# Kernel optimization log

Measured on AMD Instinct MI355X. Metric: run time of the kernel, lower is better.

## Reference

```python
import jax, jax.numpy as jnp
import numpy as np

B, T, C, H = 8, 2048, 1024, 128  # batch, seq (=block_size), n_embd, head_size


def setup_inputs() -> dict:
    key = jax.random.key(0)
    kx, kk, kq, kv = jax.random.split(key, 4)
    x = jax.random.normal(kx, (B, T, C), dtype=jnp.float32)
    # nn.Linear(n_embd, head_size, bias=False) weights, stored as (in, out) for x @ W
    s = 1.0 / np.sqrt(C)
    Wk = jax.random.normal(kk, (C, H), dtype=jnp.float32) * s
    Wq = jax.random.normal(kq, (C, H), dtype=jnp.float32) * s
    Wv = jax.random.normal(kv, (C, H), dtype=jnp.float32) * s
    return {"x": x, "Wk": Wk, "Wq": Wq, "Wv": Wv}


def reference(x, Wk, Wq, Wv):
    # x: [B, T, C]
    Bx, Tx, Cx = x.shape
    k = x @ Wk  # [B, T, H]
    q = x @ Wq  # [B, T, H]
    v = x @ Wv  # [B, T, H]
    # NOTE: source multiplies by C**0.5 (not 1/sqrt), kept faithfully
    wei = jnp.einsum("bth,bsh->bts", q, k) * (Cx ** 0.5)  # [B, T, T]
    causal = jnp.tril(jnp.ones((Tx, Tx), dtype=bool))
    wei = jnp.where(causal, wei, -jnp.inf)
    wei = jax.nn.softmax(wei, axis=-1)
    # dropout omitted (eval-mode reference)
    return wei @ v  # [B, T, H]
```

## Files before the change

kernel.cpp:

```cpp
#include <hip/hip_runtime.h>

constexpr int kB = 8;
constexpr int kT = 2048;
constexpr int kC = 1024;
constexpr int kH = 128;
constexpr int kM = kB * kT;
constexpr size_t kMH = (size_t)kM * kH;
constexpr size_t kWH = (size_t)kC * kH;

typedef __attribute__((ext_vector_type(8))) short bf16x8;
typedef __attribute__((ext_vector_type(4))) float f32x4;


__device__ inline unsigned short f2bf_rne(float f) {
    union { float f; unsigned int u; } x; x.f = f;
    unsigned int r = x.u + 0x7fff + ((x.u >> 16) & 1);
    return (unsigned short)(r >> 16);
}
__device__ inline float bf2f(unsigned short h) {
    union { float f; unsigned int u; } x; x.u = ((unsigned int)h) << 16;
    return x.f;
}
__device__ inline unsigned int pack_hi2(float a, float b) {
    return __builtin_amdgcn_perm(__float_as_uint(b), __float_as_uint(a),
                                 0x07060302u);
}
__device__ inline float hi_part(float v) {
    return __uint_as_float(__float_as_uint(v) & 0xffff0000u);
}
__device__ inline void load_lds16(const unsigned short* g, unsigned short* l) {
    __builtin_amdgcn_global_load_lds(
        (const __attribute__((address_space(1))) unsigned int*)g,
        (__attribute__((address_space(3))) unsigned int*)l, 16, 0, 0);
}
#define RAW_BARRIER()  asm volatile("s_barrier" ::: "memory")
#define WAIT_VM0()     asm volatile("s_waitcnt vmcnt(0)" ::: "memory")

__global__ __launch_bounds__(256) void prep_w(
    const float* __restrict__ Wk, const float* __restrict__ Wq,
    const float* __restrict__ Wv, unsigned short* __restrict__ ws)
{
    const int h = blockIdx.x;
    const int mat = blockIdx.y;
    const float* W = (mat == 0) ? Wq : (mat == 1) ? Wk : Wv;
    unsigned short* hi = ws + 5 * kMH + (size_t)(mat * 2) * kWH;
    unsigned short* lo = hi + kWH;

    const int k0 = threadIdx.x * 4;
    unsigned short hv[4], lv[4];
#pragma unroll
    for (int j = 0; j < 4; ++j) {
        const float f = W[(size_t)(k0 + j) * kH + h];
        hv[j] = f2bf_rne(f);
        lv[j] = f2bf_rne(f - bf2f(hv[j]));
    }
    *(uint2*)&hi[(size_t)h * kC + k0] =
        make_uint2(((unsigned)hv[1] << 16) | hv[0], ((unsigned)hv[3] << 16) | hv[2]);
    *(uint2*)&lo[(size_t)h * kC + k0] =
        make_uint2(((unsigned)lv[1] << 16) | lv[0], ((unsigned)lv[3] << 16) | lv[2]);
}

__global__ __launch_bounds__(256, 2) void qkv_mfma(
    const float* __restrict__ x, unsigned short* __restrict__ ws)
{
    __shared__ __align__(16) unsigned short lds[34816];
    unsigned short* Ahi = lds;
    unsigned short* Alo = lds + 9216;
    unsigned short* Bh  = lds + 18432;
    unsigned short* Bl  = lds + 26624;

    const int idx = blockIdx.x;
    const int tid = threadIdx.x;
    const int w = tid >> 6, lane = tid & 63;
    const int li = lane & 15, quad = lane >> 4;

    if (idx < 256) {
        const int mat = idx & 1;
        const int m0 = (idx >> 1) * 128;
        const unsigned short* wThi = ws + 5 * kMH + (size_t)(mat * 2) * kWH;
        const unsigned short* wTlo = wThi + kWH;
        const int wm = w >> 1, wn = w & 1;

        f32x4 acc[4][4];
#pragma unroll
        for (int i = 0; i < 4; ++i)
#pragma unroll
            for (int j = 0; j < 4; ++j) acc[i][j] = (f32x4){0.f, 0.f, 0.f, 0.f};

        for (int kt = 0; kt < kC; kt += 64) {
            if (kt) __syncthreads();
#pragma unroll
            for (int u = 0; u < 8; ++u) {
                const int f = u * 256 + tid;
                const int row = f >> 4, c4 = (f & 15) * 4;
                const float4 xv =
                    *(const float4*)(x + (size_t)(m0 + row) * kC + kt + c4);
                const float l0 = xv.x - hi_part(xv.x), l1 = xv.y - hi_part(xv.y);
                const float l2 = xv.z - hi_part(xv.z), l3 = xv.w - hi_part(xv.w);
                *(uint2*)&Ahi[row * 72 + c4] =
                    make_uint2(pack_hi2(xv.x, xv.y), pack_hi2(xv.z, xv.w));
                *(uint2*)&Alo[row * 72 + c4] =
                    make_uint2(pack_hi2(l0, l1), pack_hi2(l2, l3));
            }
#pragma unroll
            for (int u = 0; u < 4; ++u) {
                const int f = u * 256 + tid;
                const int row = f >> 3, p = f & 7, g = p ^ (row & 7);
                load_lds16(wThi + (size_t)row * kC + kt + g * 8, Bh + f * 8);
                load_lds16(wTlo + (size_t)row * kC + kt + g * 8, Bl + f * 8);
            }
            __syncthreads();

#pragma unroll
            for (int kc = 0; kc < 2; ++kc) {
                bf16x8 ah[4], al[4];
#pragma unroll
                for (int mt = 0; mt < 4; ++mt) {
                    const int ar = (wm * 64 + mt * 16 + li) * 72 + kc * 32 + quad * 8;
                    ah[mt] = *(const bf16x8*)&Ahi[ar];
                    al[mt] = *(const bf16x8*)&Alo[ar];
                }
#pragma unroll
                for (int nt = 0; nt < 4; ++nt) {
                    const int row = wn * 64 + nt * 16 + li;
                    const int pos = (kc * 4 + quad) ^ (li & 7);
                    const bf16x8 bh = *(const bf16x8*)&Bh[row * 64 + pos * 8];
                    const bf16x8 bl = *(const bf16x8*)&Bl[row * 64 + pos * 8];
#pragma unroll
                    for (int mt = 0; mt < 4; ++mt) {
                        acc[mt][nt] = __builtin_amdgcn_mfma_f32_16x16x32_bf16(ah[mt], bh, acc[mt][nt], 0, 0, 0);
                        acc[mt][nt] = __builtin_amdgcn_mfma_f32_16x16x32_bf16(al[mt], bh, acc[mt][nt], 0, 0, 0);
                        acc[mt][nt] = __builtin_amdgcn_mfma_f32_16x16x32_bf16(ah[mt], bl, acc[mt][nt], 0, 0, 0);
                    }
                }
            }
        }
        unsigned short* hip_ = ws + (size_t)(mat * 2) * kMH;
        unsigned short* lop  = hip_ + kMH;
        const float sc = (mat == 0) ? 32.0f : 1.0f;
#pragma unroll
        for (int mt = 0; mt < 4; ++mt)
#pragma unroll
            for (int nt = 0; nt < 4; ++nt) {
                const int col = wn * 64 + nt * 16 + li;
#pragma unroll
                for (int reg = 0; reg < 4; ++reg) {
                    const int row = m0 + wm * 64 + mt * 16 + quad * 4 + reg;
                    const float v = acc[mt][nt][reg] * sc;
                    hip_[(size_t)row * kH + col] = (unsigned short)(__float_as_uint(v) >> 16);
                    lop[(size_t)row * kH + col] =
                        (unsigned short)(__float_as_uint(v - hi_part(v)) >> 16);
                }
            }
    } else {
        const int m0 = (idx - 256) * 64;
        const unsigned short* wThi = ws + 5 * kMH + (size_t)4 * kWH;
        const int rm = w >> 1, rn = w & 1;

        f32x4 acc[2][4];
#pragma unroll
        for (int i = 0; i < 2; ++i)
#pragma unroll
            for (int j = 0; j < 4; ++j) acc[i][j] = (f32x4){0.f, 0.f, 0.f, 0.f};

        for (int kt = 0; kt < kC; kt += 64) {
            if (kt) __syncthreads();
#pragma unroll
            for (int u = 0; u < 4; ++u) {
                const int f = u * 256 + tid;
                const int row = f >> 4, c4 = (f & 15) * 4;
                const float4 xv =
                    *(const float4*)(x + (size_t)(m0 + row) * kC + kt + c4);
                unsigned short h0 = f2bf_rne(xv.x), h1 = f2bf_rne(xv.y);
                unsigned short h2 = f2bf_rne(xv.z), h3 = f2bf_rne(xv.w);
                *(uint2*)&Ahi[row * 72 + c4] =
                    make_uint2(((unsigned)h1 << 16) | h0, ((unsigned)h3 << 16) | h2);
            }
#pragma unroll
            for (int u = 0; u < 4; ++u) {
                const int f = u * 256 + tid;
                const int row = f >> 3, p = f & 7, g = p ^ (row & 7);
                load_lds16(wThi + (size_t)row * kC + kt + g * 8, Bh + f * 8);
            }
            __syncthreads();

#pragma unroll
            for (int kc = 0; kc < 2; ++kc) {
                bf16x8 a[2];
#pragma unroll
                for (int mt = 0; mt < 2; ++mt)
                    a[mt] = *(const bf16x8*)&Ahi[(rm * 32 + mt * 16 + li) * 72 + kc * 32 + quad * 8];
#pragma unroll
                for (int nt = 0; nt < 4; ++nt) {
                    const int row = rn * 64 + nt * 16 + li;
                    const int pos = (kc * 4 + quad) ^ (li & 7);
                    const bf16x8 bh = *(const bf16x8*)&Bh[row * 64 + pos * 8];
#pragma unroll
                    for (int mt = 0; mt < 2; ++mt)
                        acc[mt][nt] = __builtin_amdgcn_mfma_f32_16x16x32_bf16(a[mt], bh, acc[mt][nt], 0, 0, 0);
                }
            }
        }
        unsigned short* vt = ws + 4 * kMH;
        const int bb = m0 >> 11;
        const int t00 = m0 & (kT - 1);
#pragma unroll
        for (int mt = 0; mt < 2; ++mt)
#pragma unroll
            for (int nt = 0; nt < 4; ++nt) {
                const int h = rn * 64 + nt * 16 + li;
                ushort4 pk;
                pk.x = f2bf_rne(acc[mt][nt][0]);
                pk.y = f2bf_rne(acc[mt][nt][1]);
                pk.z = f2bf_rne(acc[mt][nt][2]);
                pk.w = f2bf_rne(acc[mt][nt][3]);
                const int t0 = t00 + rm * 32 + mt * 16 + quad * 4;
                *(ushort4*)&vt[((size_t)(bb * kH + h)) * kT + t0] = pk;
            }
    }
}

__global__ __launch_bounds__(256, 2) void attn_mfma(
    const unsigned short* __restrict__ ws, float* __restrict__ out)
{
    __shared__ __align__(16) unsigned short Kh0[64 * 128];
    __shared__ __align__(16) unsigned short Kl0[64 * 128];
    __shared__ __align__(16) unsigned short Kh1[64 * 128];
    __shared__ __align__(16) unsigned short Kl1[64 * 128];
    __shared__ __align__(16) unsigned short Ps[4][16][40];
    __shared__ __align__(16) float Ml[2][2][2][16];
    __shared__ __align__(16) unsigned short Os[2][16][136];

    const int tid = threadIdx.x;
    const int w = tid >> 6, lane = tid & 63;
    const int li = lane & 15, quad = lane >> 4;
    const int r = w >> 1, c = w & 1;

    const int idx = blockIdx.x;
    const int b = idx & 7;
    const int j = idx >> 3;
    const int qt = (j < 32) ? j : 95 - j;
    const int i0 = qt * 32;
    const int nj = (qt >> 1) + 1;

    const unsigned short* qhi = ws;
    const unsigned short* qlo = ws + kMH;
    const unsigned short* khi = ws + 2 * kMH;
    const unsigned short* klo = ws + 3 * kMH;
    const unsigned short* vt  = ws + 4 * kMH;

    bf16x8 qh[4], ql[4];
    {
        const size_t qoff = ((size_t)(b * kT + i0 + r * 16 + li)) * kH;
#pragma unroll
        for (int kc = 0; kc < 4; ++kc) {
            qh[kc] = *(const bf16x8*)(qhi + qoff + kc * 32 + quad * 8);
            ql[kc] = *(const bf16x8*)(qlo + qoff + kc * 32 + quad * 8);
        }
    }

    f32x4 o[8];
#pragma unroll
    for (int ht = 0; ht < 8; ++ht) o[ht] = (f32x4){0.f, 0.f, 0.f, 0.f};
    float m_i[4] = {-3.0e38f, -3.0e38f, -3.0e38f, -3.0e38f};
    float l_i[4] = {0.f, 0.f, 0.f, 0.f};

    auto stage = [&](int jtile, unsigned short* Kh, unsigned short* Kl) {
        const size_t kgb = ((size_t)(b * kT + jtile * 64)) * kH;
#pragma unroll
        for (int u = 0; u < 4; ++u) {
            const int f = u * 256 + tid;
            const int row = f >> 4, p = f & 15, g = p ^ (row & 15);
            load_lds16(khi + kgb + row * 128 + g * 8, Kh + f * 8);
            load_lds16(klo + kgb + row * 128 + g * 8, Kl + f * 8);
        }
    };

    auto compute = [&](int jtile, const unsigned short* Kh,
                       const unsigned short* Kl,
                       unsigned short* KhN, unsigned short* KlN) {
        bf16x8 vf[8];
#pragma unroll
        for (int ht = 0; ht < 8; ++ht)
            vf[ht] = *(const bf16x8*)(vt + (size_t)(b * kH + ht * 16 + li) * kT +
                                      jtile * 64 + c * 32 + quad * 8);
        __builtin_amdgcn_sched_barrier(0);
        if (jtile + 1 < nj) stage(jtile + 1, KhN, KlN);

        f32x4 s[2];
        s[0] = (f32x4){0.f, 0.f, 0.f, 0.f};
        s[1] = (f32x4){0.f, 0.f, 0.f, 0.f};
#pragma unroll
        for (int nt = 0; nt < 2; ++nt) {
            const int t = c * 32 + nt * 16 + li;
#pragma unroll
            for (int kc = 0; kc < 4; ++kc) {
                const int pos = (kc * 4 + quad) ^ li;
                const bf16x8 kh = *(const bf16x8*)(Kh + t * 128 + pos * 8);
                const bf16x8 kl = *(const bf16x8*)(Kl + t * 128 + pos * 8);
                s[nt] = __builtin_amdgcn_mfma_f32_16x16x32_bf16(qh[kc], kh, s[nt], 0, 0, 0);
                s[nt] = __builtin_amdgcn_mfma_f32_16x16x32_bf16(ql[kc], kh, s[nt], 0, 0, 0);
                s[nt] = __builtin_amdgcn_mfma_f32_16x16x32_bf16(qh[kc], kl, s[nt], 0, 0, 0);
            }
        }
        if (jtile == nj - 1) {
            const int grow0 = i0 + r * 16 + quad * 4;
            const int gcol0 = jtile * 64 + c * 32 + li;
#pragma unroll
            for (int nt = 0; nt < 2; ++nt)
#pragma unroll
                for (int reg = 0; reg < 4; ++reg)
                    if (gcol0 + nt * 16 > grow0 + reg) s[nt][reg] = -3.0e38f;
        }
        float alpha[4];
#pragma unroll
        for (int reg = 0; reg < 4; ++reg) {
            float mr = fmaxf(s[0][reg], s[1][reg]);
            mr = fmaxf(mr, __shfl_xor(mr, 1));
            mr = fmaxf(mr, __shfl_xor(mr, 2));
            mr = fmaxf(mr, __shfl_xor(mr, 4));
            mr = fmaxf(mr, __shfl_xor(mr, 8));
            const float mn = fmaxf(m_i[reg], mr);
            alpha[reg] = __expf(m_i[reg] - mn);
            m_i[reg] = mn;
            const float p0 = __expf(s[0][reg] - mn);
            const float p1 = __expf(s[1][reg] - mn);
            s[0][reg] = p0; s[1][reg] = p1;
            float rs = p0 + p1;
            rs += __shfl_xor(rs, 1);
            rs += __shfl_xor(rs, 2);
            rs += __shfl_xor(rs, 4);
            rs += __shfl_xor(rs, 8);
            l_i[reg] = l_i[reg] * alpha[reg] + rs;
        }
        const f32x4 av = {alpha[0], alpha[1], alpha[2], alpha[3]};
#pragma unroll
        for (int ht = 0; ht < 8; ++ht) o[ht] *= av;
#pragma unroll
        for (int nt = 0; nt < 2; ++nt)
#pragma unroll
            for (int reg = 0; reg < 4; ++reg)
                Ps[w][quad * 4 + reg][nt * 16 + li] = f2bf_rne(s[nt][reg]);
        const bf16x8 pf = *(const bf16x8*)&Ps[w][li][quad * 8];
#pragma unroll
        for (int ht = 0; ht < 8; ++ht)
            o[ht] = __builtin_amdgcn_mfma_f32_16x16x32_bf16(pf, vf[ht], o[ht], 0, 0, 0);
    };

    stage(0, Kh0, Kl0);
    int jt = 0;
    while (true) {
        WAIT_VM0();
        RAW_BARRIER();
        compute(jt, Kh0, Kl0, Kh1, Kl1);
        if (++jt >= nj) break;
        WAIT_VM0();
        RAW_BARRIER();
        compute(jt, Kh1, Kl1, Kh0, Kl0);
        if (++jt >= nj) break;
    }

    __syncthreads();
#pragma unroll
    for (int reg = 0; reg < 4; ++reg) {
        Ml[r][c][0][quad * 4 + reg] = m_i[reg];
        Ml[r][c][1][quad * 4 + reg] = l_i[reg];
    }
    __syncthreads();
    float a_self[4], linv[4];
#pragma unroll
    for (int reg = 0; reg < 4; ++reg) {
        const float mo = Ml[r][c ^ 1][0][quad * 4 + reg];
        const float lo_ = Ml[r][c ^ 1][1][quad * 4 + reg];
        const float mm = fmaxf(m_i[reg], mo);
        a_self[reg] = __expf(m_i[reg] - mm);
        const float a_oth = __expf(mo - mm);
        linv[reg] = 1.0f / (l_i[reg] * a_self[reg] + lo_ * a_oth);
    }
    if (c == 1) {
#pragma unroll
        for (int ht = 0; ht < 8; ++ht)
#pragma unroll
            for (int reg = 0; reg < 4; ++reg)
                Os[r][quad * 4 + reg][ht * 16 + li] =
                    f2bf_rne(o[ht][reg] * a_self[reg]);
    }
    __syncthreads();
    if (c == 0) {
#pragma unroll
        for (int ht = 0; ht < 8; ++ht)
#pragma unroll
            for (int reg = 0; reg < 4; ++reg) {
                const float v = o[ht][reg] * a_self[reg] +
                                bf2f(Os[r][quad * 4 + reg][ht * 16 + li]);
                out[(size_t)(b * kT + i0 + r * 16 + quad * 4 + reg) * kH +
                    ht * 16 + li] = v * linv[reg];
            }
    }
}

extern "C" void kernel_launch(void* const* d_in, const int* in_sizes, int n_in,
                              void* d_out, int out_size, void* d_ws, size_t ws_size,
                              hipStream_t stream) {
    const float* x  = (const float*)d_in[0];
    const float* Wk = (const float*)d_in[1];
    const float* Wq = (const float*)d_in[2];
    const float* Wv = (const float*)d_in[3];
    unsigned short* ws = (unsigned short*)d_ws;
    float* out = (float*)d_out;

    hipLaunchKernelGGL(prep_w, dim3(128, 3), dim3(256), 0, stream, Wk, Wq, Wv, ws);
    hipLaunchKernelGGL(qkv_mfma, dim3(512), dim3(256), 0, stream, x, ws);
    hipLaunchKernelGGL(attn_mfma, dim3(512), dim3(256), 0, stream,
                       (const unsigned short*)ws, out);
}
```

Measured before the change: 216.6 us.

## Split attention KV range across warps and unify QKV projection tiling

The attention kernel now gives each block a 16-row query tile and splits the key range across its four warps in 64-key chunks. K and V are read straight from global memory rather than staged through double-buffered LDS, and the four partial softmax states are merged at the end in fp32. Softmax moves to exp2 by folding log2(e) into the Q scale. The QKV projection uses a single 64-row tiling for all three matrices with a larger grid. This trades LDS reuse of K for more parallelism and occupancy, at the cost of redundant global K/V loads and a four-way reduction.

Result: slower. 229.7 us (+6.0%).

```diff
diff --git a/kernel.cpp b/kernel.cpp
--- a/kernel.cpp
+++ b/kernel.cpp
@@ -8,6 +8,8 @@
 constexpr size_t kMH = (size_t)kM * kH;
 constexpr size_t kWH = (size_t)kC * kH;
 
+#define QSCALE 46.166241308446828f
+
 typedef __attribute__((ext_vector_type(8))) short bf16x8;
 typedef __attribute__((ext_vector_type(4))) float f32x4;
 
@@ -33,8 +35,6 @@
         (const __attribute__((address_space(1))) unsigned int*)g,
         (__attribute__((address_space(3))) unsigned int*)l, 16, 0, 0);
 }
-#define RAW_BARRIER()  asm volatile("s_barrier" ::: "memory")
-#define WAIT_VM0()     asm volatile("s_waitcnt vmcnt(0)" ::: "memory")
 
 __global__ __launch_bounds__(256) void prep_w(
     const float* __restrict__ Wk, const float* __restrict__ Wq,
@@ -60,52 +60,52 @@
         make_uint2(((unsigned)lv[1] << 16) | lv[0], ((unsigned)lv[3] << 16) | lv[2]);
 }
 
-__global__ __launch_bounds__(256, 2) void qkv_mfma(
+__global__ __launch_bounds__(256) void qkv_mfma(
     const float* __restrict__ x, unsigned short* __restrict__ ws)
 {
-    __shared__ __align__(16) unsigned short lds[34816];
-    unsigned short* Ahi = lds;
-    unsigned short* Alo = lds + 9216;
-    unsigned short* Bh  = lds + 18432;
-    unsigned short* Bl  = lds + 26624;
+    __shared__ __align__(16) unsigned short Ah[64][72];
+    __shared__ __align__(16) unsigned short Al[64][72];
+    __shared__ __align__(16) unsigned short Bh[128 * 64];
+    __shared__ __align__(16) unsigned short Bl[128 * 64];
 
     const int idx = blockIdx.x;
+    const int mat = idx >> 8;
+    const int m0 = (idx & 255) * 64;
+    const unsigned short* wThi = ws + 5 * kMH + (size_t)(mat * 2) * kWH;
+    const unsigned short* wTlo = wThi + kWH;
+
     const int tid = threadIdx.x;
     const int w = tid >> 6, lane = tid & 63;
     const int li = lane & 15, quad = lane >> 4;
-
-    if (idx < 256) {
-        const int mat = idx & 1;
-        const int m0 = (idx >> 1) * 128;
-        const unsigned short* wThi = ws + 5 * kMH + (size_t)(mat * 2) * kWH;
-        const unsigned short* wTlo = wThi + kWH;
-        const int wm = w >> 1, wn = w & 1;
-
-        f32x4 acc[4][4];
-#pragma unroll
-        for (int i = 0; i < 4; ++i)
-#pragma unroll
-            for (int j = 0; j < 4; ++j) acc[i][j] = (f32x4){0.f, 0.f, 0.f, 0.f};
-
+    const int wm = w >> 1, wn = w & 1;
+
+    const int ar = tid >> 2;
+    const int ac = (tid & 3) * 16;
+
+    f32x4 acc[2][4];
+#pragma unroll
+    for (int i = 0; i < 2; ++i)
+#pragma unroll
+        for (int j = 0; j < 4; ++j) acc[i][j] = (f32x4){0.f, 0.f, 0.f, 0.f};
+
+    if (mat <= 1) {
         for (int kt = 0; kt < kC; kt += 64) {
             if (kt) __syncthreads();
 #pragma unroll
-            for (int u = 0; u < 8; ++u) {
-                const int f = u * 256 + tid;
-                const int row = f >> 4, c4 = (f & 15) * 4;
+            for (int u = 0; u < 4; ++u) {
                 const float4 xv =
-                    *(const float4*)(x + (size_t)(m0 + row) * kC + kt + c4);
+                    *(const float4*)(x + (size_t)(m0 + ar) * kC + kt + ac + u * 4);
                 const float l0 = xv.x - hi_part(xv.x), l1 = xv.y - hi_part(xv.y);
                 const float l2 = xv.z - hi_part(xv.z), l3 = xv.w - hi_part(xv.w);
-                *(uint2*)&Ahi[row * 72 + c4] =
+                *(uint2*)&Ah[ar][ac + u * 4] =
                     make_uint2(pack_hi2(xv.x, xv.y), pack_hi2(xv.z, xv.w));
-                *(uint2*)&Alo[row * 72 + c4] =
+                *(uint2*)&Al[ar][ac + u * 4] =
                     make_uint2(pack_hi2(l0, l1), pack_hi2(l2, l3));
             }
 #pragma unroll
             for (int u = 0; u < 4; ++u) {
                 const int f = u * 256 + tid;
-                const int row = f >> 3, p = f & 7, g = p ^ (row & 7);
+                const int row = f >> 3, g = (f & 7) ^ (row & 7);
                 load_lds16(wThi + (size_t)row * kC + kt + g * 8, Bh + f * 8);
                 load_lds16(wTlo + (size_t)row * kC + kt + g * 8, Bl + f * 8);
             }
@@ -113,21 +113,20 @@
 
 #pragma unroll
             for (int kc = 0; kc < 2; ++kc) {
-                bf16x8 ah[4], al[4];
-#pragma unroll
-                for (int mt = 0; mt < 4; ++mt) {
-                    const int ar = (wm * 64 + mt * 16 + li) * 72 + kc * 32 + quad * 8;
-                    ah[mt] = *(const bf16x8*)&Ahi[ar];
-                    al[mt] = *(const bf16x8*)&Alo[ar];
+                bf16x8 ah[2], al[2];
+#pragma unroll
+                for (int mt = 0; mt < 2; ++mt) {
+                    ah[mt] = *(const bf16x8*)&Ah[wm * 32 + mt * 16 + li][kc * 32 + quad * 8];
+                    al[mt] = *(const bf16x8*)&Al[wm * 32 + mt * 16 + li][kc * 32 + quad * 8];
                 }
 #pragma unroll
                 for (int nt = 0; nt < 4; ++nt) {
                     const int row = wn * 64 + nt * 16 + li;
-                    const int pos = (kc * 4 + quad) ^ (li & 7);
+                    const int pos = (kc * 4 + quad) ^ (row & 7);
                     const bf16x8 bh = *(const bf16x8*)&Bh[row * 64 + pos * 8];
                     const bf16x8 bl = *(const bf16x8*)&Bl[row * 64 + pos * 8];
 #pragma unroll
-                    for (int mt = 0; mt < 4; ++mt) {
+                    for (int mt = 0; mt < 2; ++mt) {
                         acc[mt][nt] = __builtin_amdgcn_mfma_f32_16x16x32_bf16(ah[mt], bh, acc[mt][nt], 0, 0, 0);
                         acc[mt][nt] = __builtin_amdgcn_mfma_f32_16x16x32_bf16(al[mt], bh, acc[mt][nt], 0, 0, 0);
                         acc[mt][nt] = __builtin_amdgcn_mfma_f32_16x16x32_bf16(ah[mt], bl, acc[mt][nt], 0, 0, 0);
@@ -137,15 +136,15 @@
         }
         unsigned short* hip_ = ws + (size_t)(mat * 2) * kMH;
         unsigned short* lop  = hip_ + kMH;
-        const float sc = (mat == 0) ? 32.0f : 1.0f;
-#pragma unroll
-        for (int mt = 0; mt < 4; ++mt)
+        const float sc = (mat == 0) ? QSCALE : 1.0f;
+#pragma unroll
+        for (int mt = 0; mt < 2; ++mt)
 #pragma unroll
             for (int nt = 0; nt < 4; ++nt) {
                 const int col = wn * 64 + nt * 16 + li;
 #pragma unroll
                 for (int reg = 0; reg < 4; ++reg) {
-                    const int row = m0 + wm * 64 + mt * 16 + quad * 4 + reg;
+                    const int row = m0 + wm * 32 + mt * 16 + quad * 4 + reg;
                     const float v = acc[mt][nt][reg] * sc;
                     hip_[(size_t)row * kH + col] = (unsigned short)(__float_as_uint(v) >> 16);
                     lop[(size_t)row * kH + col] =
@@ -153,33 +152,21 @@
                 }
             }
     } else {
-        const int m0 = (idx - 256) * 64;
-        const unsigned short* wThi = ws + 5 * kMH + (size_t)4 * kWH;
-        const int rm = w >> 1, rn = w & 1;
-
-        f32x4 acc[2][4];
-#pragma unroll
-        for (int i = 0; i < 2; ++i)
-#pragma unroll
-            for (int j = 0; j < 4; ++j) acc[i][j] = (f32x4){0.f, 0.f, 0.f, 0.f};
-
         for (int kt = 0; kt < kC; kt += 64) {
             if (kt) __syncthreads();
 #pragma unroll
             for (int u = 0; u < 4; ++u) {
-                const int f = u * 256 + tid;
-                const int row = f >> 4, c4 = (f & 15) * 4;
                 const float4 xv =
-                    *(const float4*)(x + (size_t)(m0 + row) * kC + kt + c4);
+                    *(const float4*)(x + (size_t)(m0 + ar) * kC + kt + ac + u * 4);
                 unsigned short h0 = f2bf_rne(xv.x), h1 = f2bf_rne(xv.y);
                 unsigned short h2 = f2bf_rne(xv.z), h3 = f2bf_rne(xv.w);
-                *(uint2*)&Ahi[row * 72 + c4] =
+                *(uint2*)&Ah[ar][ac + u * 4] =
                     make_uint2(((unsigned)h1 << 16) | h0, ((unsigned)h3 << 16) | h2);
             }
 #pragma unroll
             for (int u = 0; u < 4; ++u) {
                 const int f = u * 256 + tid;
-                const int row = f >> 3, p = f & 7, g = p ^ (row & 7);
+                const int row = f >> 3, g = (f & 7) ^ (row & 7);
                 load_lds16(wThi + (size_t)row * kC + kt + g * 8, Bh + f * 8);
             }
             __syncthreads();
@@ -189,11 +176,11 @@
                 bf16x8 a[2];
 #pragma unroll
                 for (int mt = 0; mt < 2; ++mt)
-                    a[mt] = *(const bf16x8*)&Ahi[(rm * 32 + mt * 16 + li) * 72 + kc * 32 + quad * 8];
+                    a[mt] = *(const bf16x8*)&Ah[wm * 32 + mt * 16 + li][kc * 32 + quad * 8];
 #pragma unroll
                 for (int nt = 0; nt < 4; ++nt) {
-                    const int row = rn * 64 + nt * 16 + li;
-                    const int pos = (kc * 4 + quad) ^ (li & 7);
+                    const int row = wn * 64 + nt * 16 + li;
+                    const int pos = (kc * 4 + quad) ^ (row & 7);
                     const bf16x8 bh = *(const bf16x8*)&Bh[row * 64 + pos * 8];
 #pragma unroll
                     for (int mt = 0; mt < 2; ++mt)
@@ -203,45 +190,40 @@
         }
         unsigned short* vt = ws + 4 * kMH;
         const int bb = m0 >> 11;
-        const int t00 = m0 & (kT - 1);
+        const int t00 = (m0 & (kT - 1)) + wm * 32;
 #pragma unroll
         for (int mt = 0; mt < 2; ++mt)
 #pragma unroll
             for (int nt = 0; nt < 4; ++nt) {
-                const int h = rn * 64 + nt * 16 + li;
+                const int h = wn * 64 + nt * 16 + li;
                 ushort4 pk;
                 pk.x = f2bf_rne(acc[mt][nt][0]);
                 pk.y = f2bf_rne(acc[mt][nt][1]);
                 pk.z = f2bf_rne(acc[mt][nt][2]);
                 pk.w = f2bf_rne(acc[mt][nt][3]);
-                const int t0 = t00 + rm * 32 + mt * 16 + quad * 4;
+                const int t0 = t00 + mt * 16 + quad * 4;
                 *(ushort4*)&vt[((size_t)(bb * kH + h)) * kT + t0] = pk;
             }
     }
 }
 
-__global__ __launch_bounds__(256, 2) void attn_mfma(
+__global__ __launch_bounds__(256, 4) void attn_mfma(
     const unsigned short* __restrict__ ws, float* __restrict__ out)
 {
-    __shared__ __align__(16) unsigned short Kh0[64 * 128];
-    __shared__ __align__(16) unsigned short Kl0[64 * 128];
-    __shared__ __align__(16) unsigned short Kh1[64 * 128];
-    __shared__ __align__(16) unsigned short Kl1[64 * 128];
-    __shared__ __align__(16) unsigned short Ps[4][16][40];
-    __shared__ __align__(16) float Ml[2][2][2][16];
-    __shared__ __align__(16) unsigned short Os[2][16][136];
+    __shared__ __align__(16) unsigned short Ps[4][16][72];
+    __shared__ __align__(16) float Ml[4][16][2];
+    __shared__ __align__(16) float Obuf[3][16][132];
 
     const int tid = threadIdx.x;
     const int w = tid >> 6, lane = tid & 63;
     const int li = lane & 15, quad = lane >> 4;
-    const int r = w >> 1, c = w & 1;
 
     const int idx = blockIdx.x;
     const int b = idx & 7;
     const int j = idx >> 3;
-    const int qt = (j < 32) ? j : 95 - j;
-    const int i0 = qt * 32;
-    const int nj = (qt >> 1) + 1;
+    const int qt = (j < 64) ? j : 191 - j;
+    const int i0 = qt * 16;
+    const int nc = (qt + 4) >> 2;
 
     const unsigned short* qhi = ws;
     const unsigned short* qlo = ws + kMH;
@@ -251,7 +233,7 @@
 
     bf16x8 qh[4], ql[4];
     {
-        const size_t qoff = ((size_t)(b * kT + i0 + r * 16 + li)) * kH;
+        const size_t qoff = ((size_t)(b * kT + i0 + li)) * kH;
 #pragma unroll
         for (int kc = 0; kc < 4; ++kc) {
             qh[kc] = *(const bf16x8*)(qhi + qoff + kc * 32 + quad * 8);
@@ -265,68 +247,52 @@
     float m_i[4] = {-3.0e38f, -3.0e38f, -3.0e38f, -3.0e38f};
     float l_i[4] = {0.f, 0.f, 0.f, 0.f};
 
-    auto stage = [&](int jtile, unsigned short* Kh, unsigned short* Kl) {
-        const size_t kgb = ((size_t)(b * kT + jtile * 64)) * kH;
-#pragma unroll
-        for (int u = 0; u < 4; ++u) {
-            const int f = u * 256 + tid;
-            const int row = f >> 4, p = f & 15, g = p ^ (row & 15);
-            load_lds16(khi + kgb + row * 128 + g * 8, Kh + f * 8);
-            load_lds16(klo + kgb + row * 128 + g * 8, Kl + f * 8);
-        }
-    };
-
-    auto compute = [&](int jtile, const unsigned short* Kh,
-                       const unsigned short* Kl,
-                       unsigned short* KhN, unsigned short* KlN) {
-        bf16x8 vf[8];
-#pragma unroll
-        for (int ht = 0; ht < 8; ++ht)
-            vf[ht] = *(const bf16x8*)(vt + (size_t)(b * kH + ht * 16 + li) * kT +
-                                      jtile * 64 + c * 32 + quad * 8);
-        __builtin_amdgcn_sched_barrier(0);
-        if (jtile + 1 < nj) stage(jtile + 1, KhN, KlN);
-
-        f32x4 s[2];
-        s[0] = (f32x4){0.f, 0.f, 0.f, 0.f};
-        s[1] = (f32x4){0.f, 0.f, 0.f, 0.f};
-#pragma unroll
-        for (int nt = 0; nt < 2; ++nt) {
-            const int t = c * 32 + nt * 16 + li;
-#pragma unroll
-            for (int kc = 0; kc < 4; ++kc) {
-                const int pos = (kc * 4 + quad) ^ li;
-                const bf16x8 kh = *(const bf16x8*)(Kh + t * 128 + pos * 8);
-                const bf16x8 kl = *(const bf16x8*)(Kl + t * 128 + pos * 8);
+    for (int jc = w; jc < nc; jc += 4) {
+        const int t0 = jc * 64;
+        f32x4 s[4];
+#pragma unroll
+        for (int nt = 0; nt < 4; ++nt) s[nt] = (f32x4){0.f, 0.f, 0.f, 0.f};
+#pragma unroll
+        for (int kc = 0; kc < 4; ++kc) {
+#pragma unroll
+            for (int nt = 0; nt < 4; ++nt) {
+                const size_t ka =
+                    ((size_t)(b * kT + t0 + nt * 16 + li)) * kH + kc * 32 + quad * 8;
+                const bf16x8 kh = *(const bf16x8*)(khi + ka);
+                const bf16x8 kl = *(const bf16x8*)(klo + ka);
                 s[nt] = __builtin_amdgcn_mfma_f32_16x16x32_bf16(qh[kc], kh, s[nt], 0, 0, 0);
                 s[nt] = __builtin_amdgcn_mfma_f32_16x16x32_bf16(ql[kc], kh, s[nt], 0, 0, 0);
                 s[nt] = __builtin_amdgcn_mfma_f32_16x16x32_bf16(qh[kc], kl, s[nt], 0, 0, 0);
             }
         }
-        if (jtile == nj - 1) {
-            const int grow0 = i0 + r * 16 + quad * 4;
-            const int gcol0 = jtile * 64 + c * 32 + li;
-#pragma unroll
-            for (int nt = 0; nt < 2; ++nt)
+        if (jc == nc - 1) {
+            const int grow0 = i0 + quad * 4;
+#pragma unroll
+            for (int nt = 0; nt < 4; ++nt) {
+                const int gcol = t0 + nt * 16 + li;
 #pragma unroll
                 for (int reg = 0; reg < 4; ++reg)
-                    if (gcol0 + nt * 16 > grow0 + reg) s[nt][reg] = -3.0e38f;
+                    if (gcol > grow0 + reg) s[nt][reg] = -3.0e38f;
+            }
         }
         float alpha[4];
 #pragma unroll
         for (int reg = 0; reg < 4; ++reg) {
-            float mr = fmaxf(s[0][reg], s[1][reg]);
+            float mr = fmaxf(fmaxf(s[0][reg], s[1][reg]), fmaxf(s[2][reg], s[3][reg]));
             mr = fmaxf(mr, __shfl_xor(mr, 1));
             mr = fmaxf(mr, __shfl_xor(mr, 2));
             mr = fmaxf(mr, __shfl_xor(mr, 4));
             mr = fmaxf(mr, __shfl_xor(mr, 8));
             const float mn = fmaxf(m_i[reg], mr);
-            alpha[reg] = __expf(m_i[reg] - mn);
+            alpha[reg] = exp2f(m_i[reg] - mn);
             m_i[reg] = mn;
-            const float p0 = __expf(s[0][reg] - mn);
-            const float p1 = __expf(s[1][reg] - mn);
-            s[0][reg] = p0; s[1][reg] = p1;
-            float rs = p0 + p1;
+            float rs = 0.f;
+#pragma unroll
+            for (int nt = 0; nt < 4; ++nt) {
+                const float p = exp2f(s[nt][reg] - mn);
+                s[nt][reg] = p;
+                rs += p;
+            }
             rs += __shfl_xor(rs, 1);
             rs += __shfl_xor(rs, 2);
             rs += __shfl_xor(rs, 4);
@@ -337,64 +303,64 @@
 #pragma unroll
         for (int ht = 0; ht < 8; ++ht) o[ht] *= av;
 #pragma unroll
-        for (int nt = 0; nt < 2; ++nt)
+        for (int nt = 0; nt < 4; ++nt)
 #pragma unroll
             for (int reg = 0; reg < 4; ++reg)
                 Ps[w][quad * 4 + reg][nt * 16 + li] = f2bf_rne(s[nt][reg]);
-        const bf16x8 pf = *(const bf16x8*)&Ps[w][li][quad * 8];
-#pragma unroll
-        for (int ht = 0; ht < 8; ++ht)
-            o[ht] = __builtin_amdgcn_mfma_f32_16x16x32_bf16(pf, vf[ht], o[ht], 0, 0, 0);
-    };
-
-    stage(0, Kh0, Kl0);
-    int jt = 0;
-    while (true) {
-        WAIT_VM0();
-        RAW_BARRIER();
-        compute(jt, Kh0, Kl0, Kh1, Kl1);
-        if (++jt >= nj) break;
-        WAIT_VM0();
-        RAW_BARRIER();
-        compute(jt, Kh1, Kl1, Kh0, Kl0);
-        if (++jt >= nj) break;
-    }
-
-    __syncthreads();
-#pragma unroll
-    for (int reg = 0; reg < 4; ++reg) {
-        Ml[r][c][0][quad * 4 + reg] = m_i[reg];
-        Ml[r][c][1][quad * 4 + reg] = l_i[reg];
+        const bf16x8 pf0 = *(const bf16x8*)&Ps[w][li][quad * 8];
+        const bf16x8 pf1 = *(const bf16x8*)&Ps[w][li][32 + quad * 8];
+#pragma unroll
+        for (int ht = 0; ht < 8; ++ht) {
+            const size_t va = (size_t)(b * kH + ht * 16 + li) * kT + t0;
+            const bf16x8 v0 = *(const bf16x8*)(vt + va + quad * 8);
+            const bf16x8 v1 = *(const bf16x8*)(vt + va + 32 + quad * 8);
+            o[ht] = __builtin_amdgcn_mfma_f32_16x16x32_bf16(pf0, v0, o[ht], 0, 0, 0);
+            o[ht] = __builtin_amdgcn_mfma_f32_16x16x32_bf16(pf1, v1, o[ht], 0, 0, 0);
+        }
+    }
+
+    if (li == 0) {
+#pragma unroll
+        for (int reg = 0; reg < 4; ++reg) {
+            Ml[w][quad * 4 + reg][0] = m_i[reg];
+            Ml[w][quad * 4 + reg][1] = l_i[reg];
+        }
     }
     __syncthreads();
     float a_self[4], linv[4];
 #pragma unroll
     for (int reg = 0; reg < 4; ++reg) {
-        const float mo = Ml[r][c ^ 1][0][quad * 4 + reg];
-        const float lo_ = Ml[r][c ^ 1][1][quad * 4 + reg];
-        const float mm = fmaxf(m_i[reg], mo);
-        a_self[reg] = __expf(m_i[reg] - mm);
-        const float a_oth = __expf(mo - mm);
-        linv[reg] = 1.0f / (l_i[reg] * a_self[reg] + lo_ * a_oth);
-    }
-    if (c == 1) {
+        const int row = quad * 4 + reg;
+        const float m0_ = Ml[0][row][0], m1 = Ml[1][row][0];
+        const float m2 = Ml[2][row][0], m3 = Ml[3][row][0];
+        const float ms = fmaxf(fmaxf(m0_, m1), fmaxf(m2, m3));
+        const float L = Ml[0][row][1] * exp2f(m0_ - ms) +
+                        Ml[1][row][1] * exp2f(m1 - ms) +
+                        Ml[2][row][1] * exp2f(m2 - ms) +
+                        Ml[3][row][1] * exp2f(m3 - ms);
+        a_self[reg] = exp2f(m_i[reg] - ms);
+        linv[reg] = 1.0f / L;
+    }
+    if (w) {
 #pragma unroll
         for (int ht = 0; ht < 8; ++ht)
 #pragma unroll
             for (int reg = 0; reg < 4; ++reg)
-                Os[r][quad * 4 + reg][ht * 16 + li] =
-                    f2bf_rne(o[ht][reg] * a_self[reg]);
+                Obuf[w - 1][quad * 4 + reg][ht * 16 + li] =
+                    o[ht][reg] * a_self[reg];
     }
     __syncthreads();
-    if (c == 0) {
+    if (w == 0) {
 #pragma unroll
         for (int ht = 0; ht < 8; ++ht)
 #pragma unroll
             for (int reg = 0; reg < 4; ++reg) {
+                const int row = quad * 4 + reg;
+                const int col = ht * 16 + li;
                 const float v = o[ht][reg] * a_self[reg] +
-                                bf2f(Os[r][quad * 4 + reg][ht * 16 + li]);
-                out[(size_t)(b * kT + i0 + r * 16 + quad * 4 + reg) * kH +
-                    ht * 16 + li] = v * linv[reg];
+                                Obuf[0][row][col] + Obuf[1][row][col] +
+                                Obuf[2][row][col];
+                out[(size_t)(b * kT + i0 + row) * kH + col] = v * linv[reg];
             }
     }
 }
@@ -410,7 +376,7 @@
     float* out = (float*)d_out;
 
     hipLaunchKernelGGL(prep_w, dim3(128, 3), dim3(256), 0, stream, Wk, Wq, Wv, ws);
-    hipLaunchKernelGGL(qkv_mfma, dim3(512), dim3(256), 0, stream, x, ws);
-    hipLaunchKernelGGL(attn_mfma, dim3(512), dim3(256), 0, stream,
+    hipLaunchKernelGGL(qkv_mfma, dim3(768), dim3(256), 0, stream, x, ws);
+    hipLaunchKernelGGL(attn_mfma, dim3(1024), dim3(256), 0, stream,
                        (const unsigned short*)ws, out);
 }
```
